# Optimization experiments

Hardware: AMD Instinct MI355X
Metric: run time of the kernel (lower is better)

The kernel has to match this reference:

```python
import jax, jax.numpy as jnp
import numpy as np

N_USER, N_TX, E = 50000, 50000, 600000
D_USER, D_TX, D_ALIGN, HID, OUT = 128, 64, 128, 256, 128


def setup_inputs() -> dict:
    key = jax.random.key(0)
    ks = jax.random.split(key, 16)
    s = 0.05
    return {
        "x_user": jax.random.normal(ks[0], (N_USER, D_USER), jnp.float32),
        "x_tx": jax.random.normal(ks[1], (N_TX, D_TX), jnp.float32),
        "edge_user_tx": jax.random.randint(ks[2], (2, E), 0, N_USER),
        "edge_tx_user": jax.random.randint(ks[3], (2, E), 0, N_TX),
        "W_align_user": jax.random.normal(ks[4], (D_USER, D_ALIGN), jnp.float32) * s,
        "b_align_user": jnp.zeros((D_ALIGN,), jnp.float32),
        "W_align_tx": jax.random.normal(ks[5], (D_TX, D_ALIGN), jnp.float32) * s,
        "b_align_tx": jnp.zeros((D_ALIGN,), jnp.float32),
        "eps_ut": jnp.zeros((), jnp.float32),
        "eps_tu": jnp.zeros((), jnp.float32),
        "W1_ut": jax.random.normal(ks[6], (D_TX + D_ALIGN, HID), jnp.float32) * s,
        "b1_ut": jnp.zeros((HID,), jnp.float32),
        "W2_ut": jax.random.normal(ks[7], (HID, OUT), jnp.float32) * s,
        "b2_ut": jnp.zeros((OUT,), jnp.float32),
        "W1_tu": jax.random.normal(ks[8], (D_USER + D_ALIGN, HID), jnp.float32) * s,
        "b1_tu": jnp.zeros((HID,), jnp.float32),
        "W2_tu": jax.random.normal(ks[9], (HID, OUT), jnp.float32) * s,
        "b2_tu": jnp.zeros((OUT,), jnp.float32),
    }


def _mlp(h, W1, b1, W2, b2):
    return jnp.maximum(h @ W1 + b1, 0.0) @ W2 + b2


def _hexgin_conv(x_src, x_dst, edge_index, W_a, b_a, eps, W1, b1, W2, b2):
    # align src features, gather along edges, scatter-sum into dst nodes
    a_src = x_src @ W_a + b_a                       # [N_src, D_ALIGN]
    msgs = a_src[edge_index[0]]                     # [E, D_ALIGN] gather
    agg = jax.ops.segment_sum(msgs, edge_index[1], num_segments=x_dst.shape[0])
    h = jnp.concatenate([(1.0 + eps) * x_dst, agg], axis=1)
    return _mlp(h, W1, b1, W2, b2)


def reference(x_user, x_tx, edge_user_tx, edge_tx_user,
              W_align_user, b_align_user, W_align_tx, b_align_tx,
              eps_ut, eps_tu,
              W1_ut, b1_ut, W2_ut, b2_ut,
              W1_tu, b1_tu, W2_tu, b2_tu):
    # relation (user, makes, tx): updates tx nodes
    out_tx = _hexgin_conv(x_user, x_tx, edge_user_tx,
                          W_align_user, b_align_user, eps_ut,
                          W1_ut, b1_ut, W2_ut, b2_ut)
    # relation (tx, to, user): updates user nodes
    out_user = _hexgin_conv(x_tx, x_user, edge_tx_user,
                            W_align_tx, b_align_tx, eps_tu,
                            W1_tu, b1_tu, W2_tu, b2_tu)
    # HeteroConv aggr='sum': single relation per target, so plain outputs
    return out_user, out_tx
```

## Files before the change

kernel.cpp:

```cpp
#include <hip/hip_runtime.h>
#include <hip/hip_bf16.h>


#define D_USER 128
#define D_TX 64
#define D_ALIGN 128
#define HID 256
#define OUT_D 128
#define NNODE 50000
#define BI 32
#define MAXSLOT 62
#define HPAD 264

typedef __attribute__((ext_vector_type(8))) short short8;
typedef __attribute__((ext_vector_type(4))) float f32x4;
typedef unsigned short ush;

__device__ __forceinline__ ush f2bf(float f) {
    union { float f; unsigned u; } v; v.f = f;
    unsigned u = v.u + 0x7fffu + ((v.u >> 16) & 1u);
    return (ush)(u >> 16);
}
__device__ __forceinline__ float2 bfu2f(unsigned u) {
    union { unsigned u; float f; } a, b;
    a.u = (u & 0xffffu) << 16;
    b.u = u & 0xffff0000u;
    return make_float2(a.f, b.f);
}
__device__ __forceinline__ unsigned f2bfu(float2 v) {
    return (unsigned)f2bf(v.x) | ((unsigned)f2bf(v.y) << 16);
}
__device__ __forceinline__ uint4 scale_bf8(uint4 v, float e) {
    unsigned* w = (unsigned*)&v;
    #pragma unroll
    for (int t = 0; t < 4; ++t) {
        float2 f = bfu2f(w[t]);
        w[t] = f2bfu(make_float2(f.x * e, f.y * e));
    }
    return v;
}


__device__ __forceinline__ void dev_fill(const int* __restrict__ e, int E, int i,
                                         int* __restrict__ pad, int dbase)
{
    int d = dbase + e[E + i];
    int s = e[i];
    int pos = atomicAdd(&pad[(size_t)d * BI], 1);
    if (pos < MAXSLOT)
        ((ush*)pad)[(size_t)d * (2 * BI) + 2 + pos] = (ush)s;
}

__device__ __forceinline__ void dev_prep(int b, int tid,
    const float* __restrict__ xu, ush* __restrict__ xbu,
    const float* __restrict__ xt, ush* __restrict__ xbt, int n8u, int n8t,
    const float* __restrict__ Wa_u, const float* __restrict__ ba_u,
    const float* __restrict__ W1_ut,
    const float* __restrict__ Wa_t, const float* __restrict__ ba_t,
    const float* __restrict__ W1_tu,
    const float* __restrict__ W2_ut, const float* __restrict__ W2_tu,
    ush* __restrict__ Bt1a, float* __restrict__ bfv1,
    ush* __restrict__ Bt1b, float* __restrict__ bfv2,
    ush* __restrict__ Bt2a, ush* __restrict__ Bt2b, int gb)
{
    if (b < gb) {
        int i = b * 256 + tid;
        const float* x; ush* xb; int j;
        if (i < n8u) { x = xu; xb = xbu; j = i; }
        else if (i < n8u + n8t) { x = xt; xb = xbt; j = i - n8u; }
        else return;
        const float4 a = *reinterpret_cast<const float4*>(&x[(size_t)j * 8]);
        const float4 c = *reinterpret_cast<const float4*>(&x[(size_t)j * 8 + 4]);
        ush o[8];
        o[0] = f2bf(a.x); o[1] = f2bf(a.y); o[2] = f2bf(a.z); o[3] = f2bf(a.w);
        o[4] = f2bf(c.x); o[5] = f2bf(c.y); o[6] = f2bf(c.z); o[7] = f2bf(c.w);
        *reinterpret_cast<uint4*>(&xb[(size_t)j * 8]) = *reinterpret_cast<uint4*>(o);
        return;
    }
    int idx = (b - gb) * 256 + tid;
    const int KT = 192;
    const int SEG1 = HID * (KT + 1);
    const int SEG2 = OUT_D * HID;
    if (idx < 2 * SEG1) {
        bool r2 = idx >= SEG1;
        int id = r2 ? idx - SEG1 : idx;
        const float* Wa = r2 ? Wa_t : Wa_u;
        const float* ba = r2 ? ba_t : ba_u;
        const float* W1 = r2 ? W1_tu : W1_ut;
        ush* Bt = r2 ? Bt1b : Bt1a;
        float* bfv = r2 ? bfv2 : bfv1;
        const int Dd = r2 ? 128 : 64;
        int c = id & (HID - 1);
        int k = id >> 8;
        const float* w1bot = W1 + (size_t)Dd * HID;
        if (k < Dd) {
            Bt[(size_t)c * KT + k] = f2bf(W1[(size_t)k * HID + c]);
        } else if (k < KT) {
            int ks = k - Dd;
            float acc = 0.f;
            for (int j = 0; j < D_ALIGN; ++j)
                acc += Wa[ks * D_ALIGN + j] * w1bot[(size_t)j * HID + c];
            Bt[(size_t)c * KT + k] = f2bf(acc);
        } else {
            float acc = 0.f;
            for (int j = 0; j < D_ALIGN; ++j)
                acc += ba[j] * w1bot[(size_t)j * HID + c];
            bfv[c] = acc;
        }
    } else if (idx < 2 * SEG1 + 2 * SEG2) {
        int id = idx - 2 * SEG1;
        bool r2 = id >= SEG2;
        if (r2) id -= SEG2;
        const float* W2 = r2 ? W2_tu : W2_ut;
        ush* Bt2 = r2 ? Bt2b : Bt2a;
        int c = id & (OUT_D - 1);
        int k = id >> 7;
        Bt2[(size_t)c * HID + k] = f2bf(W2[(size_t)k * OUT_D + c]);
    }
}

__device__ __forceinline__ int slot_word(const int* blk, int lane)
{
    return ((lane & 31) < 31) ? blk[1 + (lane & 31)] : 0;
}
__device__ __forceinline__ int slot_get(int word, int j)
{
    return (j & 1) ? ((word >> 16) & 0xffff) : (word & 0xffff);
}

__device__ __forceinline__ void dev_agg128(int w, int lane,
    const ush* __restrict__ xbu, const int* __restrict__ pad, ush* __restrict__ Sb1)
{
    const int* blk = pad + (size_t)w * BI;
    const int n = min(blk[0], MAXSLOT);
    const int word = slot_word(blk, lane);
    float2 acc = make_float2(0.f, 0.f);
    int i = 0;
    for (; i + 4 <= n; i += 4) {
        int wa = __shfl(word, i >> 1);
        int wb = __shfl(word, (i >> 1) + 1);
        int s0 = wa & 0xffff, s1 = (wa >> 16) & 0xffff;
        int s2 = wb & 0xffff, s3 = (wb >> 16) & 0xffff;
        unsigned v0 = *reinterpret_cast<const unsigned*>(&xbu[(size_t)s0 * 128 + 2 * lane]);
        unsigned v1 = *reinterpret_cast<const unsigned*>(&xbu[(size_t)s1 * 128 + 2 * lane]);
        unsigned v2 = *reinterpret_cast<const unsigned*>(&xbu[(size_t)s2 * 128 + 2 * lane]);
        unsigned v3 = *reinterpret_cast<const unsigned*>(&xbu[(size_t)s3 * 128 + 2 * lane]);
        float2 f0 = bfu2f(v0), f1 = bfu2f(v1), f2 = bfu2f(v2), f3 = bfu2f(v3);
        acc.x += (f0.x + f1.x) + (f2.x + f3.x);
        acc.y += (f0.y + f1.y) + (f2.y + f3.y);
    }
    for (; i < n; ++i) {
        int ww = __shfl(word, i >> 1);
        int s0 = slot_get(ww, i);
        unsigned v0 = *reinterpret_cast<const unsigned*>(&xbu[(size_t)s0 * 128 + 2 * lane]);
        float2 f0 = bfu2f(v0);
        acc.x += f0.x; acc.y += f0.y;
    }
    *reinterpret_cast<unsigned*>(&Sb1[(size_t)w * 128 + 2 * lane]) = f2bfu(acc);
}

__device__ __forceinline__ void dev_agg64(int w2, int lane,
    const ush* __restrict__ xbt, const int* __restrict__ pad, ush* __restrict__ Sb2)
{
    const int* blk = pad + (size_t)(NNODE + w2) * BI;
    const int n = min(blk[0], MAXSLOT);
    const int word = slot_word(blk, lane);
    const int half = lane >> 5, l2 = lane & 31;
    float2 acc = make_float2(0.f, 0.f);
    int i = 0;
    for (; i + 4 <= n; i += 4) {
        int ja = i + half, jb = i + 2 + half;
        int wa = __shfl(word, ja >> 1);
        int wb = __shfl(word, jb >> 1);
        int s0 = slot_get(wa, ja), s1 = slot_get(wb, jb);
        unsigned v0 = *reinterpret_cast<const unsigned*>(&xbt[(size_t)s0 * 64 + 2 * l2]);
        unsigned v1 = *reinterpret_cast<const unsigned*>(&xbt[(size_t)s1 * 64 + 2 * l2]);
        float2 f0 = bfu2f(v0), f1 = bfu2f(v1);
        acc.x += f0.x + f1.x;
        acc.y += f0.y + f1.y;
    }
    for (; i + 2 <= n; i += 2) {
        int j = i + half;
        int ww = __shfl(word, j >> 1);
        int s0 = slot_get(ww, j);
        unsigned v0 = *reinterpret_cast<const unsigned*>(&xbt[(size_t)s0 * 64 + 2 * l2]);
        float2 f0 = bfu2f(v0);
        acc.x += f0.x; acc.y += f0.y;
    }
    if (i < n && half == 0) {
        int ww = __shfl(word, i >> 1);
        int s0 = slot_get(ww, i);
        unsigned v0 = *reinterpret_cast<const unsigned*>(&xbt[(size_t)s0 * 64 + 2 * l2]);
        float2 f0 = bfu2f(v0);
        acc.x += f0.x; acc.y += f0.y;
    }
    acc.x += __shfl_xor(acc.x, 32);
    acc.y += __shfl_xor(acc.y, 32);
    if (half == 0)
        *reinterpret_cast<unsigned*>(&Sb2[(size_t)w2 * 64 + 2 * l2]) = f2bfu(acc);
}


__global__ __launch_bounds__(256) void kA(
    const int* __restrict__ e_ut, int E, int* __restrict__ pad,
    const float* __restrict__ xu, ush* __restrict__ xbu,
    const float* __restrict__ xt, ush* __restrict__ xbt, int n8u, int n8t,
    const float* __restrict__ Wa_u, const float* __restrict__ ba_u,
    const float* __restrict__ W1_ut,
    const float* __restrict__ Wa_t, const float* __restrict__ ba_t,
    const float* __restrict__ W1_tu,
    const float* __restrict__ W2_ut, const float* __restrict__ W2_tu,
    ush* __restrict__ Bt1a, float* __restrict__ bfv1,
    ush* __restrict__ Bt1b, float* __restrict__ bfv2,
    ush* __restrict__ Bt2a, ush* __restrict__ Bt2b, int gf, int gb)
{
    int b = blockIdx.x, tid = threadIdx.x;
    if (b < gf) {
        int i = b * 256 + tid;
        if (i < E) dev_fill(e_ut, E, i, pad, 0);
    } else {
        dev_prep(b - gf, tid, xu, xbu, xt, xbt, n8u, n8t,
                 Wa_u, ba_u, W1_ut, Wa_t, ba_t, W1_tu, W2_ut, W2_tu,
                 Bt1a, bfv1, Bt1b, bfv2, Bt2a, Bt2b, gb);
    }
}

__global__ __launch_bounds__(256) void kB(
    const int* __restrict__ e_tu, int E, int* __restrict__ pad,
    const ush* __restrict__ xbu, ush* __restrict__ Sb1, int gf)
{
    int b = blockIdx.x, tid = threadIdx.x;
    if (b < gf) {
        int i = b * 256 + tid;
        if (i < E) dev_fill(e_tu, E, i, pad, NNODE);
    } else {
        int w = (b - gf) * 4 + (tid >> 6);
        if (w < NNODE) dev_agg128(w, tid & 63, xbu, pad, Sb1);
    }
}

__global__ __launch_bounds__(256) void kC(
    const ush* __restrict__ xbt, const int* __restrict__ pad, ush* __restrict__ Sb2)
{
    int w2 = blockIdx.x * 4 + (threadIdx.x >> 6);
    if (w2 < NNODE) dev_agg64(w2, threadIdx.x & 63, xbt, pad, Sb2);
}

__global__ __launch_bounds__(256) void mlpF(
    const ush* __restrict__ xbt, const ush* __restrict__ xbu,
    const ush* __restrict__ Sb1, const ush* __restrict__ Sb2,
    const ush* __restrict__ Bt1a, const ush* __restrict__ Bt1b,
    const float* __restrict__ bfv1, const float* __restrict__ bfv2,
    const float* __restrict__ b1_ut, const float* __restrict__ b1_tu,
    const ush* __restrict__ Bt2a, const ush* __restrict__ Bt2b,
    const float* __restrict__ b2_ut, const float* __restrict__ b2_tu,
    const int* __restrict__ pad,
    const float* __restrict__ eps_ut, const float* __restrict__ eps_tu,
    float* __restrict__ out_tx, float* __restrict__ out_user, int M)
{
    __shared__ ush As[64 * 40];
    __shared__ ush Bs[256 * 40];
    __shared__ ush Hs[64 * HPAD];

    const int tid = threadIdx.x;
    const bool r2 = blockIdx.y != 0;
    const int bm = blockIdx.x * 64;
    const ush* xdst = r2 ? xbu : xbt;
    const int Dd = r2 ? 128 : 64;
    const ush* Sb = r2 ? Sb2 : Sb1;
    const int Dsrc = r2 ? 64 : 128;
    const ush* Bt1 = r2 ? Bt1b : Bt1a;
    const float* bfv = r2 ? bfv2 : bfv1;
    const float* b1 = r2 ? b1_tu : b1_ut;
    const ush* Bt2 = r2 ? Bt2b : Bt2a;
    const float* b2 = r2 ? b2_tu : b2_ut;
    const int* dgp = pad + (size_t)(r2 ? NNODE : 0) * BI;
    float* out = r2 ? out_user : out_tx;
    const float e = 1.f + (r2 ? eps_tu[0] : eps_ut[0]);

    const int lane = tid & 63, wn = tid >> 6;
    const int lo = lane & 15, hi = lane >> 4;

    f32x4 acc[4][4];
    #pragma unroll
    for (int a = 0; a < 4; ++a)
        #pragma unroll
        for (int b = 0; b < 4; ++b)
            acc[a][b] = f32x4{0.f, 0.f, 0.f, 0.f};

    const int KT1 = 192;
    for (int k0 = 0; k0 < KT1; k0 += 32) {
        {
            int r = tid >> 2, c8 = tid & 3;
            int gr = bm + r;
            const ush* src; int ld; int kb; bool sc;
            if (k0 < Dd) { src = xdst; ld = Dd; kb = k0; sc = true; }
            else         { src = Sb;   ld = Dsrc; kb = k0 - Dd; sc = false; }
            uint4 v = uint4{0u, 0u, 0u, 0u};
            if (gr < M)
                v = *reinterpret_cast<const uint4*>(&src[(size_t)gr * ld + kb + c8 * 8]);
            if (sc) v = scale_bf8(v, e);
            *reinterpret_cast<uint4*>(&As[r * 40 + c8 * 8]) = v;
        }
        #pragma unroll
        for (int q = 0; q < 4; ++q) {
            int idx = tid + 256 * q;
            int c = idx >> 2, ku = idx & 3;
            uint4 v = *reinterpret_cast<const uint4*>(&Bt1[(size_t)c * KT1 + k0 + ku * 8]);
            *reinterpret_cast<uint4*>(&Bs[c * 40 + ku * 8]) = v;
        }
        __syncthreads();
        short8 av[4], bv[4];
        #pragma unroll
        for (int fi = 0; fi < 4; ++fi)
            av[fi] = *reinterpret_cast<const short8*>(&Bs[(wn * 64 + fi * 16 + lo) * 40 + hi * 8]);
        #pragma unroll
        for (int fj = 0; fj < 4; ++fj)
            bv[fj] = *reinterpret_cast<const short8*>(&As[(fj * 16 + lo) * 40 + hi * 8]);
        #pragma unroll
        for (int fi = 0; fi < 4; ++fi)
            #pragma unroll
            for (int fj = 0; fj < 4; ++fj)
                acc[fi][fj] = __builtin_amdgcn_mfma_f32_16x16x32_bf16(av[fi], bv[fj], acc[fi][fj], 0, 0, 0);
        __syncthreads();
    }

    #pragma unroll
    for (int fi = 0; fi < 4; ++fi) {
        int colb = wn * 64 + fi * 16 + hi * 4;
        float4 b1v = *reinterpret_cast<const float4*>(&b1[colb]);
        float4 bfl = *reinterpret_cast<const float4*>(&bfv[colb]);
        #pragma unroll
        for (int fj = 0; fj < 4; ++fj) {
            int r = fj * 16 + lo;
            int gr = bm + r;
            float dgv = (gr < M) ? (float)dgp[(size_t)gr * BI] : 0.f;
            float v0 = fmaxf(acc[fi][fj][0] + b1v.x + dgv * bfl.x, 0.f);
            float v1 = fmaxf(acc[fi][fj][1] + b1v.y + dgv * bfl.y, 0.f);
            float v2 = fmaxf(acc[fi][fj][2] + b1v.z + dgv * bfl.z, 0.f);
            float v3 = fmaxf(acc[fi][fj][3] + b1v.w + dgv * bfl.w, 0.f);
            uint2 u;
            u.x = f2bfu(make_float2(v0, v1));
            u.y = f2bfu(make_float2(v2, v3));
            *reinterpret_cast<uint2*>(&Hs[r * HPAD + colb]) = u;
        }
    }

    f32x4 acc2[2][4];
    #pragma unroll
    for (int a = 0; a < 2; ++a)
        #pragma unroll
        for (int b = 0; b < 4; ++b)
            acc2[a][b] = f32x4{0.f, 0.f, 0.f, 0.f};

    for (int k0 = 0; k0 < HID; k0 += 32) {
        #pragma unroll
        for (int q = 0; q < 2; ++q) {
            int idx = tid + 256 * q;
            int c = idx >> 2, ku = idx & 3;
            uint4 v = *reinterpret_cast<const uint4*>(&Bt2[(size_t)c * HID + k0 + ku * 8]);
            *reinterpret_cast<uint4*>(&Bs[c * 40 + ku * 8]) = v;
        }
        __syncthreads();
        short8 av2[2], bv2[4];
        #pragma unroll
        for (int fi = 0; fi < 2; ++fi)
            av2[fi] = *reinterpret_cast<const short8*>(&Bs[(wn * 32 + fi * 16 + lo) * 40 + hi * 8]);
        #pragma unroll
        for (int fj = 0; fj < 4; ++fj)
            bv2[fj] = *reinterpret_cast<const short8*>(&Hs[(fj * 16 + lo) * HPAD + k0 + hi * 8]);
        #pragma unroll
        for (int fi = 0; fi < 2; ++fi)
            #pragma unroll
            for (int fj = 0; fj < 4; ++fj)
                acc2[fi][fj] = __builtin_amdgcn_mfma_f32_16x16x32_bf16(av2[fi], bv2[fj], acc2[fi][fj], 0, 0, 0);
        __syncthreads();
    }

    #pragma unroll
    for (int fi = 0; fi < 2; ++fi) {
        int colb = wn * 32 + fi * 16 + hi * 4;
        float4 b2v = *reinterpret_cast<const float4*>(&b2[colb]);
        #pragma unroll
        for (int fj = 0; fj < 4; ++fj) {
            int gr = bm + fj * 16 + lo;
            if (gr >= M) continue;
            float4 o;
            o.x = acc2[fi][fj][0] + b2v.x;
            o.y = acc2[fi][fj][1] + b2v.y;
            o.z = acc2[fi][fj][2] + b2v.z;
            o.w = acc2[fi][fj][3] + b2v.w;
            *reinterpret_cast<float4*>(&out[(size_t)gr * OUT_D + colb]) = o;
        }
    }
}

extern "C" void kernel_launch(void* const* d_in, const int* in_sizes, int n_in,
                              void* d_out, int out_size, void* d_ws, size_t ws_size,
                              hipStream_t stream)
{
    const float* x_user   = (const float*)d_in[0];
    const float* x_tx     = (const float*)d_in[1];
    const int*   e_ut     = (const int*)d_in[2];
    const int*   e_tu     = (const int*)d_in[3];
    const float* Wa_user  = (const float*)d_in[4];
    const float* ba_user  = (const float*)d_in[5];
    const float* Wa_tx    = (const float*)d_in[6];
    const float* ba_tx    = (const float*)d_in[7];
    const float* eps_ut   = (const float*)d_in[8];
    const float* eps_tu   = (const float*)d_in[9];
    const float* W1_ut    = (const float*)d_in[10];
    const float* b1_ut    = (const float*)d_in[11];
    const float* W2_ut    = (const float*)d_in[12];
    const float* b2_ut    = (const float*)d_in[13];
    const float* W1_tu    = (const float*)d_in[14];
    const float* b1_tu    = (const float*)d_in[15];
    const float* W2_tu    = (const float*)d_in[16];
    const float* b2_tu    = (const float*)d_in[17];

    const int N_user = in_sizes[0] / D_USER;
    const int N_tx   = in_sizes[1] / D_TX;
    const int E      = in_sizes[2] / 2;
    const int NT     = 2 * NNODE;

    float* out_user = (float*)d_out;
    float* out_tx   = (float*)d_out + (size_t)N_user * OUT_D;

    int*   pad   = (int*)d_ws;
    float* fws   = (float*)d_ws;
    ush*   Bt1a  = (ush*)(fws + 3300000);
    ush*   Bt1b  = (ush*)(fws + 3330000);
    ush*   Bt2a  = (ush*)(fws + 3360000);
    ush*   Bt2b  = (ush*)(fws + 3380000);
    float* bfv1  = fws + 3400000;
    float* bfv2  = fws + 3401000;
    ush*   xbu   = (ush*)(fws + 3410000);
    ush*   xbt   = (ush*)(fws + 6700000);
    ush*   Sb1   = (ush*)(fws + 8400000);
    ush*   Sb2   = (ush*)(fws + 11700000);

    const int threads = 256;
    const int n8u = N_user * D_USER / 8, n8t = N_tx * D_TX / 8;
    const int gf  = (E + 255) / 256;
    const int gb  = (n8u + n8t + 255) / 256;
    const int gw  = (2 * HID * 193 + 2 * OUT_D * HID + 255) / 256;
    const int ga  = (NNODE + 3) / 4;
    const int nbF = (NNODE + 63) / 64;

    hipMemsetAsync(pad, 0, (size_t)NT * BI * sizeof(int), stream);

    kA<<<gf + gb + gw, threads, 0, stream>>>(
        e_ut, E, pad, x_user, xbu, x_tx, xbt, n8u, n8t,
        Wa_user, ba_user, W1_ut, Wa_tx, ba_tx, W1_tu, W2_ut, W2_tu,
        Bt1a, bfv1, Bt1b, bfv2, Bt2a, Bt2b, gf, gb);

    kB<<<gf + ga, threads, 0, stream>>>(e_tu, E, pad, xbu, Sb1, gf);

    kC<<<ga, threads, 0, stream>>>(xbt, pad, Sb2);

    dim3 gF(nbF, 2);
    mlpF<<<gF, threads, 0, stream>>>(
        xbt, xbu, Sb1, Sb2, Bt1a, Bt1b, bfv1, bfv2, b1_ut, b1_tu,
        Bt2a, Bt2b, b2_ut, b2_tu, pad, eps_ut, eps_tu,
        out_tx, out_user, NNODE);
}
```

Baseline: 187.3 us.

## Load MLP GEMM operands directly from global into registers, drop LDS staging

```diff
diff --git a/kernel.cpp b/kernel.cpp
--- a/kernel.cpp
+++ b/kernel.cpp
@@ -258,8 +258,6 @@
     const float* __restrict__ eps_ut, const float* __restrict__ eps_tu,
     float* __restrict__ out_tx, float* __restrict__ out_user, int M)
 {
-    __shared__ ush As[64 * 40];
-    __shared__ ush Bs[256 * 40];
     __shared__ ush Hs[64 * HPAD];
 
     const int tid = threadIdx.x;
@@ -290,39 +288,27 @@
 
     const int KT1 = 192;
     for (int k0 = 0; k0 < KT1; k0 += 32) {
-        {
-            int r = tid >> 2, c8 = tid & 3;
-            int gr = bm + r;
-            const ush* src; int ld; int kb; bool sc;
-            if (k0 < Dd) { src = xdst; ld = Dd; kb = k0; sc = true; }
-            else         { src = Sb;   ld = Dsrc; kb = k0 - Dd; sc = false; }
-            uint4 v = uint4{0u, 0u, 0u, 0u};
-            if (gr < M)
-                v = *reinterpret_cast<const uint4*>(&src[(size_t)gr * ld + kb + c8 * 8]);
+        const ush* src; int ld; int kb; bool sc;
+        if (k0 < Dd) { src = xdst; ld = Dd; kb = k0; sc = true; }
+        else         { src = Sb;   ld = Dsrc; kb = k0 - Dd; sc = false; }
+        short8 bv[4];
+        #pragma unroll
+        for (int fj = 0; fj < 4; ++fj) {
+            int row = min(bm + fj * 16 + lo, M - 1);
+            uint4 v = *reinterpret_cast<const uint4*>(&src[(size_t)row * ld + kb + hi * 8]);
             if (sc) v = scale_bf8(v, e);
-            *reinterpret_cast<uint4*>(&As[r * 40 + c8 * 8]) = v;
+            bv[fj] = *reinterpret_cast<short8*>(&v);
         }
-        #pragma unroll
-        for (int q = 0; q < 4; ++q) {
-            int idx = tid + 256 * q;
-            int c = idx >> 2, ku = idx & 3;
-            uint4 v = *reinterpret_cast<const uint4*>(&Bt1[(size_t)c * KT1 + k0 + ku * 8]);
-            *reinterpret_cast<uint4*>(&Bs[c * 40 + ku * 8]) = v;
-        }
-        __syncthreads();
-        short8 av[4], bv[4];
+        short8 av[4];
         #pragma unroll
         for (int fi = 0; fi < 4; ++fi)
-            av[fi] = *reinterpret_cast<const short8*>(&Bs[(wn * 64 + fi * 16 + lo) * 40 + hi * 8]);
-        #pragma unroll
-        for (int fj = 0; fj < 4; ++fj)
-            bv[fj] = *reinterpret_cast<const short8*>(&As[(fj * 16 + lo) * 40 + hi * 8]);
+            av[fi] = *reinterpret_cast<const short8*>(
+                &Bt1[(size_t)(wn * 64 + fi * 16 + lo) * KT1 + k0 + hi * 8]);
         #pragma unroll
         for (int fi = 0; fi < 4; ++fi)
             #pragma unroll
             for (int fj = 0; fj < 4; ++fj)
                 acc[fi][fj] = __builtin_amdgcn_mfma_f32_16x16x32_bf16(av[fi], bv[fj], acc[fi][fj], 0, 0, 0);
-        __syncthreads();
     }
 
     #pragma unroll
@@ -346,6 +332,8 @@
         }
     }
 
+    __syncthreads();
+
     f32x4 acc2[2][4];
     #pragma unroll
     for (int a = 0; a < 2; ++a)
@@ -354,18 +342,11 @@
             acc2[a][b] = f32x4{0.f, 0.f, 0.f, 0.f};
 
     for (int k0 = 0; k0 < HID; k0 += 32) {
-        #pragma unroll
-        for (int q = 0; q < 2; ++q) {
-            int idx = tid + 256 * q;
-            int c = idx >> 2, ku = idx & 3;
-            uint4 v = *reinterpret_cast<const uint4*>(&Bt2[(size_t)c * HID + k0 + ku * 8]);
-            *reinterpret_cast<uint4*>(&Bs[c * 40 + ku * 8]) = v;
-        }
-        __syncthreads();
         short8 av2[2], bv2[4];
         #pragma unroll
         for (int fi = 0; fi < 2; ++fi)
-            av2[fi] = *reinterpret_cast<const short8*>(&Bs[(wn * 32 + fi * 16 + lo) * 40 + hi * 8]);
+            av2[fi] = *reinterpret_cast<const short8*>(
+                &Bt2[(size_t)(wn * 32 + fi * 16 + lo) * HID + k0 + hi * 8]);
         #pragma unroll
         for (int fj = 0; fj < 4; ++fj)
             bv2[fj] = *reinterpret_cast<const short8*>(&Hs[(fj * 16 + lo) * HPAD + k0 + hi * 8]);
@@ -374,7 +355,6 @@
             #pragma unroll
             for (int fj = 0; fj < 4; ++fj)
                 acc2[fi][fj] = __builtin_amdgcn_mfma_f32_16x16x32_bf16(av2[fi], bv2[fj], acc2[fi][fj], 0, 0, 0);
-        __syncthreads();
     }
 
     #pragma unroll
```

Result: slower. 204.7 us (+9.2%).

## Double-buffer LDS tiles in fused MLP kernel with register prefetch

Applied to the files above, without the earlier changes.

```diff
diff --git a/kernel.cpp b/kernel.cpp
--- a/kernel.cpp
+++ b/kernel.cpp
@@ -258,9 +258,11 @@
     const float* __restrict__ eps_ut, const float* __restrict__ eps_tu,
     float* __restrict__ out_tx, float* __restrict__ out_user, int M)
 {
-    __shared__ ush As[64 * 40];
-    __shared__ ush Bs[256 * 40];
-    __shared__ ush Hs[64 * HPAD];
+    __shared__ ush lds[30720];
+    ush* BsBuf[2] = { lds,         lds + 10240 };
+    ush* AsBuf[2] = { lds + 20480, lds + 23040 };
+    ush* Hs       = lds;
+    ush* B2Buf[2] = { lds + 20480, lds + 25600 };
 
     const int tid = threadIdx.x;
     const bool r2 = blockIdx.y != 0;
@@ -280,6 +282,40 @@
 
     const int lane = tid & 63, wn = tid >> 6;
     const int lo = lane & 15, hi = lane >> 4;
+    const int KT1 = 192;
+
+    auto loadA = [&](int k0x) -> uint4 {
+        const ush* src; int ld, kb; bool sc;
+        if (k0x < Dd) { src = xdst; ld = Dd; kb = k0x; sc = true; }
+        else          { src = Sb;   ld = Dsrc; kb = k0x - Dd; sc = false; }
+        int r = tid >> 2, c8 = tid & 3;
+        int gr = bm + r;
+        uint4 v = uint4{0u, 0u, 0u, 0u};
+        if (gr < M)
+            v = *reinterpret_cast<const uint4*>(&src[(size_t)gr * ld + kb + c8 * 8]);
+        if (sc) v = scale_bf8(v, e);
+        return v;
+    };
+    auto storeA = [&](ush* dst, uint4 v) {
+        int r = tid >> 2, c8 = tid & 3;
+        *reinterpret_cast<uint4*>(&dst[r * 40 + c8 * 8]) = v;
+    };
+    auto loadB = [&](int k0x, uint4* o) {
+        #pragma unroll
+        for (int q = 0; q < 4; ++q) {
+            int idx = tid + 256 * q;
+            int c = idx >> 2, ku = idx & 3;
+            o[q] = *reinterpret_cast<const uint4*>(&Bt1[(size_t)c * KT1 + k0x + ku * 8]);
+        }
+    };
+    auto storeB = [&](ush* dst, const uint4* o) {
+        #pragma unroll
+        for (int q = 0; q < 4; ++q) {
+            int idx = tid + 256 * q;
+            int c = idx >> 2, ku = idx & 3;
+            *reinterpret_cast<uint4*>(&dst[c * 40 + ku * 8]) = o[q];
+        }
+    };
 
     f32x4 acc[4][4];
     #pragma unroll
@@ -288,40 +324,38 @@
         for (int b = 0; b < 4; ++b)
             acc[a][b] = f32x4{0.f, 0.f, 0.f, 0.f};
 
-    const int KT1 = 192;
-    for (int k0 = 0; k0 < KT1; k0 += 32) {
-        {
-            int r = tid >> 2, c8 = tid & 3;
-            int gr = bm + r;
-            const ush* src; int ld; int kb; bool sc;
-            if (k0 < Dd) { src = xdst; ld = Dd; kb = k0; sc = true; }
-            else         { src = Sb;   ld = Dsrc; kb = k0 - Dd; sc = false; }
-            uint4 v = uint4{0u, 0u, 0u, 0u};
-            if (gr < M)
-                v = *reinterpret_cast<const uint4*>(&src[(size_t)gr * ld + kb + c8 * 8]);
-            if (sc) v = scale_bf8(v, e);
-            *reinterpret_cast<uint4*>(&As[r * 40 + c8 * 8]) = v;
-        }
-        #pragma unroll
-        for (int q = 0; q < 4; ++q) {
-            int idx = tid + 256 * q;
-            int c = idx >> 2, ku = idx & 3;
-            uint4 v = *reinterpret_cast<const uint4*>(&Bt1[(size_t)c * KT1 + k0 + ku * 8]);
-            *reinterpret_cast<uint4*>(&Bs[c * 40 + ku * 8]) = v;
-        }
-        __syncthreads();
+    {
+        uint4 a0 = loadA(0);
+        uint4 b0[4]; loadB(0, b0);
+        storeA(AsBuf[0], a0);
+        storeB(BsBuf[0], b0);
+    }
+    __syncthreads();
+
+    for (int k = 0; k < 6; ++k) {
+        ush* Ac = AsBuf[k & 1];
+        ush* Bc = BsBuf[k & 1];
+        uint4 a_pf; uint4 b_pf[4];
+        if (k < 5) {
+            a_pf = loadA((k + 1) * 32);
+            loadB((k + 1) * 32, b_pf);
+        }
         short8 av[4], bv[4];
         #pragma unroll
         for (int fi = 0; fi < 4; ++fi)
-            av[fi] = *reinterpret_cast<const short8*>(&Bs[(wn * 64 + fi * 16 + lo) * 40 + hi * 8]);
+            av[fi] = *reinterpret_cast<const short8*>(&Bc[(wn * 64 + fi * 16 + lo) * 40 + hi * 8]);
         #pragma unroll
         for (int fj = 0; fj < 4; ++fj)
-            bv[fj] = *reinterpret_cast<const short8*>(&As[(fj * 16 + lo) * 40 + hi * 8]);
+            bv[fj] = *reinterpret_cast<const short8*>(&Ac[(fj * 16 + lo) * 40 + hi * 8]);
         #pragma unroll
         for (int fi = 0; fi < 4; ++fi)
             #pragma unroll
             for (int fj = 0; fj < 4; ++fj)
                 acc[fi][fj] = __builtin_amdgcn_mfma_f32_16x16x32_bf16(av[fi], bv[fj], acc[fi][fj], 0, 0, 0);
+        if (k < 5) {
+            storeA(AsBuf[(k + 1) & 1], a_pf);
+            storeB(BsBuf[(k + 1) & 1], b_pf);
+        }
         __syncthreads();
     }
 
@@ -346,6 +380,23 @@
         }
     }
 
+    auto loadB2 = [&](int k0x, uint4* o) {
+        #pragma unroll
+        for (int q = 0; q < 2; ++q) {
+            int idx = tid + 256 * q;
+            int c = idx >> 2, ku = idx & 3;
+            o[q] = *reinterpret_cast<const uint4*>(&Bt2[(size_t)c * HID + k0x + ku * 8]);
+        }
+    };
+    auto storeB2 = [&](ush* dst, const uint4* o) {
+        #pragma unroll
+        for (int q = 0; q < 2; ++q) {
+            int idx = tid + 256 * q;
+            int c = idx >> 2, ku = idx & 3;
+            *reinterpret_cast<uint4*>(&dst[c * 40 + ku * 8]) = o[q];
+        }
+    };
+
     f32x4 acc2[2][4];
     #pragma unroll
     for (int a = 0; a < 2; ++a)
@@ -353,27 +404,29 @@
         for (int b = 0; b < 4; ++b)
             acc2[a][b] = f32x4{0.f, 0.f, 0.f, 0.f};
 
-    for (int k0 = 0; k0 < HID; k0 += 32) {
-        #pragma unroll
-        for (int q = 0; q < 2; ++q) {
-            int idx = tid + 256 * q;
-            int c = idx >> 2, ku = idx & 3;
-            uint4 v = *reinterpret_cast<const uint4*>(&Bt2[(size_t)c * HID + k0 + ku * 8]);
-            *reinterpret_cast<uint4*>(&Bs[c * 40 + ku * 8]) = v;
-        }
-        __syncthreads();
+    {
+        uint4 c0[2]; loadB2(0, c0);
+        storeB2(B2Buf[0], c0);
+    }
+    __syncthreads();
+
+    for (int k = 0; k < 8; ++k) {
+        ush* Cc = B2Buf[k & 1];
+        uint4 c_pf[2];
+        if (k < 7) loadB2((k + 1) * 32, c_pf);
         short8 av2[2], bv2[4];
         #pragma unroll
         for (int fi = 0; fi < 2; ++fi)
-            av2[fi] = *reinterpret_cast<const short8*>(&Bs[(wn * 32 + fi * 16 + lo) * 40 + hi * 8]);
+            av2[fi] = *reinterpret_cast<const short8*>(&Cc[(wn * 32 + fi * 16 + lo) * 40 + hi * 8]);
         #pragma unroll
         for (int fj = 0; fj < 4; ++fj)
-            bv2[fj] = *reinterpret_cast<const short8*>(&Hs[(fj * 16 + lo) * HPAD + k0 + hi * 8]);
+            bv2[fj] = *reinterpret_cast<const short8*>(&Hs[(fj * 16 + lo) * HPAD + k * 32 + hi * 8]);
         #pragma unroll
         for (int fi = 0; fi < 2; ++fi)
             #pragma unroll
             for (int fj = 0; fj < 4; ++fj)
                 acc2[fi][fj] = __builtin_amdgcn_mfma_f32_16x16x32_bf16(av2[fi], bv2[fj], acc2[fi][fj], 0, 0, 0);
+        if (k < 7) storeB2(B2Buf[(k + 1) & 1], c_pf);
         __syncthreads();
     }
 
```

After: 205.7 us. 9.8% more time.

## Double-buffer LDS tiles with register prefetch in fused MLP kernel

Applied to the files above, without the earlier changes.

```diff
diff --git a/kernel.cpp b/kernel.cpp
--- a/kernel.cpp
+++ b/kernel.cpp
@@ -258,9 +258,7 @@
     const float* __restrict__ eps_ut, const float* __restrict__ eps_tu,
     float* __restrict__ out_tx, float* __restrict__ out_user, int M)
 {
-    __shared__ ush As[64 * 40];
-    __shared__ ush Bs[256 * 40];
-    __shared__ ush Hs[64 * HPAD];
+    __shared__ ush lds[27136];
 
     const int tid = threadIdx.x;
     const bool r2 = blockIdx.y != 0;
@@ -280,6 +278,10 @@
 
     const int lane = tid & 63, wn = tid >> 6;
     const int lo = lane & 15, hi = lane >> 4;
+    const int KT1 = 192;
+
+    const int sA_r = tid >> 2, sA_c8 = tid & 3;
+    const int sB_c0 = tid >> 2, sB_ku = tid & 3;
 
     f32x4 acc[4][4];
     #pragma unroll
@@ -288,40 +290,70 @@
         for (int b = 0; b < 4; ++b)
             acc[a][b] = f32x4{0.f, 0.f, 0.f, 0.f};
 
-    const int KT1 = 192;
-    for (int k0 = 0; k0 < KT1; k0 += 32) {
-        {
-            int r = tid >> 2, c8 = tid & 3;
-            int gr = bm + r;
-            const ush* src; int ld; int kb; bool sc;
-            if (k0 < Dd) { src = xdst; ld = Dd; kb = k0; sc = true; }
-            else         { src = Sb;   ld = Dsrc; kb = k0 - Dd; sc = false; }
-            uint4 v = uint4{0u, 0u, 0u, 0u};
+    {
+        const ush* src; int ld, kb;
+        if (0 < Dd) { src = xdst; ld = Dd; kb = 0; }
+        int gr = bm + sA_r;
+        uint4 va = uint4{0u, 0u, 0u, 0u};
+        if (gr < M)
+            va = *reinterpret_cast<const uint4*>(&src[(size_t)gr * ld + kb + sA_c8 * 8]);
+        va = scale_bf8(va, e);
+        *reinterpret_cast<uint4*>(&lds[20480 + sA_r * 40 + sA_c8 * 8]) = va;
+        #pragma unroll
+        for (int q = 0; q < 4; ++q) {
+            int c = sB_c0 + 64 * q;
+            uint4 v = *reinterpret_cast<const uint4*>(&Bt1[(size_t)c * KT1 + sB_ku * 8]);
+            *reinterpret_cast<uint4*>(&lds[c * 40 + sB_ku * 8]) = v;
+        }
+    }
+    __syncthreads();
+
+    #pragma unroll
+    for (int k = 0; k < 6; ++k) {
+        const int pOff  = (k & 1) ? 10240 : 0;
+        const int pAOff = (k & 1) ? 23040 : 20480;
+        const int nOff  = (k & 1) ? 0 : 10240;
+        const int nAOff = (k & 1) ? 20480 : 23040;
+
+        uint4 a_pf; uint4 b_pf[4];
+        if (k < 5) {
+            const int k0n = (k + 1) * 32;
+            const ush* src; int ld, kb; bool sc;
+            if (k0n < Dd) { src = xdst; ld = Dd; kb = k0n; sc = true; }
+            else          { src = Sb;   ld = Dsrc; kb = k0n - Dd; sc = false; }
+            int gr = bm + sA_r;
+            a_pf = uint4{0u, 0u, 0u, 0u};
             if (gr < M)
-                v = *reinterpret_cast<const uint4*>(&src[(size_t)gr * ld + kb + c8 * 8]);
-            if (sc) v = scale_bf8(v, e);
-            *reinterpret_cast<uint4*>(&As[r * 40 + c8 * 8]) = v;
-        }
-        #pragma unroll
-        for (int q = 0; q < 4; ++q) {
-            int idx = tid + 256 * q;
-            int c = idx >> 2, ku = idx & 3;
-            uint4 v = *reinterpret_cast<const uint4*>(&Bt1[(size_t)c * KT1 + k0 + ku * 8]);
-            *reinterpret_cast<uint4*>(&Bs[c * 40 + ku * 8]) = v;
-        }
-        __syncthreads();
+                a_pf = *reinterpret_cast<const uint4*>(&src[(size_t)gr * ld + kb + sA_c8 * 8]);
+            if (sc) a_pf = scale_bf8(a_pf, e);
+            #pragma unroll
+            for (int q = 0; q < 4; ++q) {
+                int c = sB_c0 + 64 * q;
+                b_pf[q] = *reinterpret_cast<const uint4*>(&Bt1[(size_t)c * KT1 + k0n + sB_ku * 8]);
+            }
+        }
+
         short8 av[4], bv[4];
         #pragma unroll
         for (int fi = 0; fi < 4; ++fi)
-            av[fi] = *reinterpret_cast<const short8*>(&Bs[(wn * 64 + fi * 16 + lo) * 40 + hi * 8]);
+            av[fi] = *reinterpret_cast<const short8*>(&lds[pOff + (wn * 64 + fi * 16 + lo) * 40 + hi * 8]);
         #pragma unroll
         for (int fj = 0; fj < 4; ++fj)
-            bv[fj] = *reinterpret_cast<const short8*>(&As[(fj * 16 + lo) * 40 + hi * 8]);
+            bv[fj] = *reinterpret_cast<const short8*>(&lds[pAOff + (fj * 16 + lo) * 40 + hi * 8]);
         #pragma unroll
         for (int fi = 0; fi < 4; ++fi)
             #pragma unroll
             for (int fj = 0; fj < 4; ++fj)
                 acc[fi][fj] = __builtin_amdgcn_mfma_f32_16x16x32_bf16(av[fi], bv[fj], acc[fi][fj], 0, 0, 0);
+
+        if (k < 5) {
+            *reinterpret_cast<uint4*>(&lds[nAOff + sA_r * 40 + sA_c8 * 8]) = a_pf;
+            #pragma unroll
+            for (int q = 0; q < 4; ++q) {
+                int c = sB_c0 + 64 * q;
+                *reinterpret_cast<uint4*>(&lds[nOff + c * 40 + sB_ku * 8]) = b_pf[q];
+            }
+        }
         __syncthreads();
     }
 
@@ -342,7 +374,7 @@
             uint2 u;
             u.x = f2bfu(make_float2(v0, v1));
             u.y = f2bfu(make_float2(v2, v3));
-            *reinterpret_cast<uint2*>(&Hs[r * HPAD + colb]) = u;
+            *reinterpret_cast<uint2*>(&lds[r * HPAD + colb]) = u;
         }
     }
 
@@ -353,27 +385,51 @@
         for (int b = 0; b < 4; ++b)
             acc2[a][b] = f32x4{0.f, 0.f, 0.f, 0.f};
 
-    for (int k0 = 0; k0 < HID; k0 += 32) {
+    {
         #pragma unroll
         for (int q = 0; q < 2; ++q) {
-            int idx = tid + 256 * q;
-            int c = idx >> 2, ku = idx & 3;
-            uint4 v = *reinterpret_cast<const uint4*>(&Bt2[(size_t)c * HID + k0 + ku * 8]);
-            *reinterpret_cast<uint4*>(&Bs[c * 40 + ku * 8]) = v;
-        }
-        __syncthreads();
+            int c = sB_c0 + 64 * q;
+            uint4 v = *reinterpret_cast<const uint4*>(&Bt2[(size_t)c * HID + sB_ku * 8]);
+            *reinterpret_cast<uint4*>(&lds[16896 + c * 40 + sB_ku * 8]) = v;
+        }
+    }
+    __syncthreads();
+
+    #pragma unroll
+    for (int k = 0; k < 8; ++k) {
+        const int pOff = (k & 1) ? 22016 : 16896;
+        const int nOff = (k & 1) ? 16896 : 22016;
+
+        uint4 c_pf[2];
+        if (k < 7) {
+            const int k0n = (k + 1) * 32;
+            #pragma unroll
+            for (int q = 0; q < 2; ++q) {
+                int c = sB_c0 + 64 * q;
+                c_pf[q] = *reinterpret_cast<const uint4*>(&Bt2[(size_t)c * HID + k0n + sB_ku * 8]);
+            }
+        }
+
         short8 av2[2], bv2[4];
         #pragma unroll
         for (int fi = 0; fi < 2; ++fi)
-            av2[fi] = *reinterpret_cast<const short8*>(&Bs[(wn * 32 + fi * 16 + lo) * 40 + hi * 8]);
+            av2[fi] = *reinterpret_cast<const short8*>(&lds[pOff + (wn * 32 + fi * 16 + lo) * 40 + hi * 8]);
         #pragma unroll
         for (int fj = 0; fj < 4; ++fj)
-            bv2[fj] = *reinterpret_cast<const short8*>(&Hs[(fj * 16 + lo) * HPAD + k0 + hi * 8]);
+            bv2[fj] = *reinterpret_cast<const short8*>(&lds[(fj * 16 + lo) * HPAD + k * 32 + hi * 8]);
         #pragma unroll
         for (int fi = 0; fi < 2; ++fi)
             #pragma unroll
             for (int fj = 0; fj < 4; ++fj)
                 acc2[fi][fj] = __builtin_amdgcn_mfma_f32_16x16x32_bf16(av2[fi], bv2[fj], acc2[fi][fj], 0, 0, 0);
+
+        if (k < 7) {
+            #pragma unroll
+            for (int q = 0; q < 2; ++q) {
+                int c = sB_c0 + 64 * q;
+                *reinterpret_cast<uint4*>(&lds[nOff + c * 40 + sB_ku * 8]) = c_pf[q];
+            }
+        }
         __syncthreads();
     }
 
```

Result: no change. 184.6 us, median of 2 (-1.5%).
